# Optimization experiments

Measured on AMD Instinct MI355X. Metric: run time of the kernel, lower is better.

Reference implementation:

```python
import jax, jax.numpy as jnp
import numpy as np

N_NODES = 20000
N_EDGES = 640000
IN_FEAT = 128
OUT_FEAT = 128
NUM_RELS = 16


def setup_inputs() -> dict:
    key = jax.random.key(0)
    k_h, k_w, k_n, k_s, k_d, k_r = jax.random.split(key, 6)
    h = jax.random.normal(k_h, (N_NODES, IN_FEAT), dtype=jnp.float32)
    weight = jax.random.normal(k_w, (NUM_RELS, IN_FEAT, OUT_FEAT), dtype=jnp.float32)
    norm = jax.random.uniform(k_n, (N_EDGES, 1), dtype=jnp.float32)
    src = jax.random.randint(k_s, (N_EDGES,), 0, N_NODES, dtype=jnp.int32)
    dst = jax.random.randint(k_d, (N_EDGES,), 0, N_NODES, dtype=jnp.int32)
    rel_type = jax.random.randint(k_r, (N_EDGES,), 0, NUM_RELS, dtype=jnp.int32)
    return {"h": h, "weight": weight, "norm": norm,
            "src": src, "dst": dst, "rel_type": rel_type}


def reference(h, weight, norm, src, dst, rel_type):
    # Math of the non-input-layer path:
    #   msg_e = (h[src_e] @ weight[rel_e]) * norm_e ; h'_v = relu(sum_{e: dst_e=v} msg_e)
    # Efficient form: project node features through every relation once
    # (R*N*d*d flops, avoids materializing [E, d, d] gathered weights),
    # then gather the (rel, src) projection per edge.
    proj = jnp.einsum('nd,rde->rne', h, weight)      # [R, N, out]
    msg = proj[rel_type, src] * norm                 # [E, out]
    agg = jax.ops.segment_sum(msg, dst, num_segments=h.shape[0])  # [N, out]
    return jax.nn.relu(agg)
```

## Files before the change

### kernel.cpp

```cpp
#include <hip/hip_runtime.h>
#include <hip/hip_bf16.h>

#define FEAT 128
#define NRELS 16
#define BKT_SZ 32
#define PCHUNK 2048
#define CAP 2048

using short8 = __attribute__((ext_vector_type(8))) short;
using f32x4  = __attribute__((ext_vector_type(4))) float;

__device__ inline ushort f2bf(float x) {
    union { float f; unsigned int u; } v; v.f = x;
    unsigned int u = v.u;
    unsigned int r = (u + 0x7fffu + ((u >> 16) & 1u)) >> 16;
    return (ushort)r;
}
__device__ inline float bf2f(ushort b) {
    union { unsigned int u; float f; } v; v.u = ((unsigned int)b) << 16;
    return v.f;
}

__global__ __launch_bounds__(256) void prep_kernel(
    const float* __restrict__ h, const float* __restrict__ W,
    ushort* __restrict__ hpack, ushort* __restrict__ wpack,
    int* __restrict__ gcur,
    int n_nodes, int nmblk, int nbkt)
{
    const int bid = blockIdx.x;
    if (bid < nmblk) {
        int t = bid * 256 + threadIdx.x;
        int lane = t & 63;
        int mblk = t >> 8;
        int ks   = (t >> 6) & 3;
        int row  = mblk * 16 + (lane & 15);
        int k0   = ks * 32 + (lane >> 4) * 8;

        ushort u[8] = {0, 0, 0, 0, 0, 0, 0, 0};
        if (row < n_nodes) {
            const float* p = h + (size_t)row * FEAT + k0;
            float4 a = *reinterpret_cast<const float4*>(p);
            float4 b = *reinterpret_cast<const float4*>(p + 4);
            u[0] = f2bf(a.x); u[1] = f2bf(a.y); u[2] = f2bf(a.z); u[3] = f2bf(a.w);
            u[4] = f2bf(b.x); u[5] = f2bf(b.y); u[6] = f2bf(b.z); u[7] = f2bf(b.w);
        }
        *reinterpret_cast<short8*>(hpack + (size_t)t * 8) = *reinterpret_cast<short8*>(u);
    } else if (bid < nmblk + 128) {
        int t = (bid - nmblk) * 256 + threadIdx.x;
        int lane = t & 63;
        int ks   = (t >> 6) & 3;
        int fb   = (t >> 8) & 7;
        int r    = t >> 11;
        int k0   = ks * 32 + (lane >> 4) * 8;
        int f    = fb * 16 + (lane & 15);

        ushort u[8];
        #pragma unroll
        for (int j = 0; j < 8; ++j)
            u[j] = f2bf(W[((size_t)r * FEAT + (k0 + j)) * FEAT + f]);
        *reinterpret_cast<short8*>(wpack + (size_t)t * 8) = *reinterpret_cast<short8*>(u);
    } else {
        for (int i = threadIdx.x; i < nbkt + 1; i += 256) gcur[i] = 0;
    }
}

__global__ __launch_bounds__(256) void fused2_kernel(
    const ushort* __restrict__ hpack, const ushort* __restrict__ wpack,
    ushort* __restrict__ proj,
    const int* __restrict__ src, const int* __restrict__ dst,
    const int* __restrict__ rel, const float* __restrict__ norm,
    int* __restrict__ gcur, uint2* __restrict__ rtmp, int* __restrict__ ovf,
    int n_nodes, int nmblk, int n_edges, int nbkt, int nchunks)
{
    __shared__ __align__(16) char smem[32768];

    if ((int)blockIdx.x < nchunks) {
        int*    cnt   = (int*)smem;
        int*    base  = cnt + 1024;
        int*    cur   = base + 1024;
        uint2*  stage = (uint2*)(cur + 1024);
        ushort* sbkt  = (ushort*)(stage + PCHUNK);

        const int tid = threadIdx.x;
        const int c0 = blockIdx.x * PCHUNK;
        int* ovf_cnt = gcur + nbkt;

        for (int i = tid; i < nbkt; i += 256) { cnt[i] = 0; cur[i] = 0; }
        __syncthreads();

        #pragma unroll
        for (int j = 0; j < PCHUNK / 256; ++j) {
            int slot = j * 256 + tid;
            int e = c0 + slot;
            if (e < n_edges) {
                int d = dst[e];
                int b = d >> 5;
                uint2 r;
                r.x = (unsigned)src[e] | ((unsigned)rel[e] << 15) | ((unsigned)(d & 31) << 19);
                r.y = __float_as_uint(norm[e]);
                stage[slot] = r;
                sbkt[slot] = (ushort)b;
                atomicAdd(&cnt[b], 1);
            } else {
                sbkt[slot] = 0xffffu;
            }
        }
        __syncthreads();

        for (int i = tid; i < nbkt; i += 256)
            if (cnt[i] > 0) base[i] = atomicAdd(&gcur[i], cnt[i]);
        __syncthreads();

        #pragma unroll
        for (int j = 0; j < PCHUNK / 256; ++j) {
            int slot = j * 256 + tid;
            ushort b = sbkt[slot];
            if (b != 0xffffu) {
                int rank = atomicAdd(&cur[b], 1);
                int pos = base[b] + rank;
                if (pos < CAP)
                    rtmp[(size_t)b * CAP + pos] = stage[slot];
                else
                    ovf[atomicAdd(ovf_cnt, 1)] = c0 + slot;
            }
        }
    } else {
        const int bid2 = (int)blockIdx.x - nchunks;
        const int rr   = bid2 >> 7;
        const int bx   = bid2 & 127;

        const int lane = threadIdx.x & 63;
        const int wv   = threadIdx.x >> 6;
        ushort (*S)[136] = reinterpret_cast<ushort(*)[136]>(smem + wv * (16 * 136 * 2));

        const short8* wp = reinterpret_cast<const short8*>(wpack);
        const short8* hp = reinterpret_cast<const short8*>(hpack);

        short8 X[8][4];
        #pragma unroll
        for (int fb = 0; fb < 8; ++fb)
            #pragma unroll
            for (int ks = 0; ks < 4; ++ks)
                X[fb][ks] = wp[(((rr * 8 + fb) * 4 + ks) << 6) + lane];

        const int niter = (nmblk + 3) / 4;

        for (int it = bx; it < niter; it += 128) {
            const int mb = it * 4 + wv;
            const bool active = (mb < nmblk);

            f32x4 acc[8];
            #pragma unroll
            for (int fb = 0; fb < 8; ++fb) acc[fb] = f32x4{0.f, 0.f, 0.f, 0.f};

            if (active) {
                short8 Y[4];
                #pragma unroll
                for (int ks = 0; ks < 4; ++ks)
                    Y[ks] = hp[((mb * 4 + ks) << 6) + lane];

                #pragma unroll
                for (int ks = 0; ks < 4; ++ks)
                    #pragma unroll
                    for (int fb = 0; fb < 8; ++fb)
                        acc[fb] = __builtin_amdgcn_mfma_f32_16x16x32_bf16(X[fb][ks], Y[ks], acc[fb], 0, 0, 0);
            }

            __syncthreads();

            if (active) {
                #pragma unroll
                for (int fb = 0; fb < 8; ++fb) {
                    uint2 d;
                    d.x = (unsigned)f2bf(acc[fb][0]) | ((unsigned)f2bf(acc[fb][1]) << 16);
                    d.y = (unsigned)f2bf(acc[fb][2]) | ((unsigned)f2bf(acc[fb][3]) << 16);
                    *reinterpret_cast<uint2*>(&S[lane & 15][fb * 16 + (lane >> 4) * 4]) = d;
                }
            }

            __syncthreads();

            if (active) {
                #pragma unroll
                for (int i = 0; i < 4; ++i) {
                    const int row  = i * 4 + (lane >> 4);
                    const int node = mb * 16 + row;
                    if (node < n_nodes) {
                        uint4 v = *reinterpret_cast<const uint4*>(&S[row][(lane & 15) * 8]);
                        *reinterpret_cast<uint4*>(
                            proj + ((size_t)rr * n_nodes + node) * FEAT + (lane & 15) * 8) = v;
                    }
                }
            }
        }
    }
}

__global__ __launch_bounds__(512) void bgather_kernel(
    const ushort* __restrict__ proj, const uint2* __restrict__ rtmp,
    const int* __restrict__ gcur, const int* __restrict__ ovf,
    const int* __restrict__ src, const int* __restrict__ dst,
    const int* __restrict__ rel, const float* __restrict__ norm,
    float* __restrict__ out, int n_nodes, int nbkt)
{
    __shared__ uint2 stage[CAP];
    __shared__ uint2 sorted[CAP];
    __shared__ int cnt[BKT_SZ], cur[BKT_SZ], nbeg[BKT_SZ];

    const int b   = blockIdx.x;
    const int tid = threadIdx.x;
    const uint2* slab = rtmp + (size_t)b * CAP;

    const int total = gcur[b];
    const int n = (total < CAP) ? total : CAP;

    if (tid < BKT_SZ) cnt[tid] = 0;
    __syncthreads();
    for (int i = tid; i < n; i += 512) {
        uint2 r = slab[i];
        stage[i] = r;
        atomicAdd(&cnt[(r.x >> 19) & 31u], 1);
    }
    __syncthreads();
    if (tid == 0) {
        int run = 0;
        for (int k = 0; k < BKT_SZ; ++k) { nbeg[k] = run; cur[k] = run; run += cnt[k]; }
    }
    __syncthreads();
    for (int i = tid; i < n; i += 512) {
        uint2 r = stage[i];
        int p = atomicAdd(&cur[(r.x >> 19) & 31u], 1);
        sorted[p] = r;
    }
    __syncthreads();

    const int lane = tid & 63;
    const int wv   = tid >> 6;
    const int grp  = lane >> 4;
    const int sl   = lane & 15;
    const int k    = wv * 4 + grp;
    const int node = b * BKT_SZ + k;
    if (node >= n_nodes) return;

    float a0 = 0.f, a1 = 0.f, a2 = 0.f, a3 = 0.f;
    float a4 = 0.f, a5 = 0.f, a6 = 0.f, a7 = 0.f;

    const int s0 = nbeg[k];
    const int s1 = s0 + cnt[k];

    uint4 va, vb, vc;
    unsigned nm0 = 0, nm1 = 0, nm2 = 0;
    va = vb = vc = make_uint4(0u, 0u, 0u, 0u);
    if (s0 < s1) {
        uint2 r = sorted[s0]; nm0 = r.y;
        va = *reinterpret_cast<const uint4*>(proj +
            ((size_t)((r.x >> 15) & 0xfu) * n_nodes + (r.x & 0x7fffu)) * FEAT + sl * 8);
    }
    if (s0 + 1 < s1) {
        uint2 r = sorted[s0 + 1]; nm1 = r.y;
        vb = *reinterpret_cast<const uint4*>(proj +
            ((size_t)((r.x >> 15) & 0xfu) * n_nodes + (r.x & 0x7fffu)) * FEAT + sl * 8);
    }
    if (s0 + 2 < s1) {
        uint2 r = sorted[s0 + 2]; nm2 = r.y;
        vc = *reinterpret_cast<const uint4*>(proj +
            ((size_t)((r.x >> 15) & 0xfu) * n_nodes + (r.x & 0x7fffu)) * FEAT + sl * 8);
    }

    for (int s = s0; s < s1; ++s) {
        uint4 vcur = va; unsigned nmu = nm0;
        va = vb; nm0 = nm1;
        vb = vc; nm1 = nm2;
        if (s + 3 < s1) {
            uint2 r = sorted[s + 3]; nm2 = r.y;
            vc = *reinterpret_cast<const uint4*>(proj +
                ((size_t)((r.x >> 15) & 0xfu) * n_nodes + (r.x & 0x7fffu)) * FEAT + sl * 8);
        }
        float nmc = __uint_as_float(nmu);
        a0 += bf2f((ushort)(vcur.x & 0xffffu)) * nmc;
        a1 += bf2f((ushort)(vcur.x >> 16)) * nmc;
        a2 += bf2f((ushort)(vcur.y & 0xffffu)) * nmc;
        a3 += bf2f((ushort)(vcur.y >> 16)) * nmc;
        a4 += bf2f((ushort)(vcur.z & 0xffffu)) * nmc;
        a5 += bf2f((ushort)(vcur.z >> 16)) * nmc;
        a6 += bf2f((ushort)(vcur.w & 0xffffu)) * nmc;
        a7 += bf2f((ushort)(vcur.w >> 16)) * nmc;
    }

    const int novf = gcur[nbkt];
    for (int i = 0; i < novf; ++i) {
        int e = ovf[i];
        if (dst[e] == node) {
            float nmc = norm[e];
            const ushort* prow = proj +
                ((size_t)rel[e] * n_nodes + src[e]) * FEAT + sl * 8;
            uint4 v = *reinterpret_cast<const uint4*>(prow);
            a0 += bf2f((ushort)(v.x & 0xffffu)) * nmc;
            a1 += bf2f((ushort)(v.x >> 16)) * nmc;
            a2 += bf2f((ushort)(v.y & 0xffffu)) * nmc;
            a3 += bf2f((ushort)(v.y >> 16)) * nmc;
            a4 += bf2f((ushort)(v.z & 0xffffu)) * nmc;
            a5 += bf2f((ushort)(v.z >> 16)) * nmc;
            a6 += bf2f((ushort)(v.w & 0xffffu)) * nmc;
            a7 += bf2f((ushort)(v.w >> 16)) * nmc;
        }
    }

    float* o = out + (size_t)node * FEAT + sl * 8;
    float4 o0, o1;
    o0.x = fmaxf(a0, 0.f); o0.y = fmaxf(a1, 0.f);
    o0.z = fmaxf(a2, 0.f); o0.w = fmaxf(a3, 0.f);
    o1.x = fmaxf(a4, 0.f); o1.y = fmaxf(a5, 0.f);
    o1.z = fmaxf(a6, 0.f); o1.w = fmaxf(a7, 0.f);
    *reinterpret_cast<float4*>(o)     = o0;
    *reinterpret_cast<float4*>(o + 4) = o1;
}

constexpr int BM = 64;

__global__ __launch_bounds__(256) void proj_kernel(
    const float* __restrict__ h, const float* __restrict__ W,
    ushort* __restrict__ proj, int n_nodes, int r0)
{
    __shared__ ushort Wt[128][136];
    __shared__ ushort hs[BM][136];

    const int tid  = threadIdx.x;
    const int rel  = r0 + blockIdx.y;
    const float* Wg = W + (size_t)rel * FEAT * FEAT;

    #pragma unroll
    for (int it = 0; it < 16; ++it) {
        int f = (it * 256 + tid) * 4;
        int k = f >> 7, n = f & 127;
        float4 w4 = *reinterpret_cast<const float4*>(Wg + f);
        Wt[n + 0][k] = f2bf(w4.x);
        Wt[n + 1][k] = f2bf(w4.y);
        Wt[n + 2][k] = f2bf(w4.z);
        Wt[n + 3][k] = f2bf(w4.w);
    }

    const int lane = tid & 63;
    const int wave = tid >> 6;
    const int r    = lane & 15;
    const int kgrp = lane >> 4;

    ushort* projr = proj + (size_t)blockIdx.y * n_nodes * FEAT;
    const int nchunks = (n_nodes + BM - 1) / BM;

    for (int c = blockIdx.x; c < nchunks; c += gridDim.x) {
        const int m0 = c * BM;
        __syncthreads();
        #pragma unroll
        for (int it = 0; it < 8; ++it) {
            int f = (it * 256 + tid) * 4;
            int m = f >> 7, k = f & 127;
            int row = m0 + m;
            float4 v = make_float4(0.f, 0.f, 0.f, 0.f);
            if (row < n_nodes)
                v = *reinterpret_cast<const float4*>(h + (size_t)row * FEAT + k);
            ushort4 u;
            u.x = f2bf(v.x); u.y = f2bf(v.y); u.z = f2bf(v.z); u.w = f2bf(v.w);
            *reinterpret_cast<ushort4*>(&hs[m][k]) = u;
        }
        __syncthreads();

        f32x4 acc[8];
        #pragma unroll
        for (int i = 0; i < 8; ++i) acc[i] = f32x4{0.f, 0.f, 0.f, 0.f};

        #pragma unroll
        for (int kk = 0; kk < 4; ++kk) {
            const int kbase = kk * 32 + kgrp * 8;
            short8 a = *reinterpret_cast<const short8*>(&hs[wave * 16 + r][kbase]);
            #pragma unroll
            for (int ct = 0; ct < 8; ++ct) {
                short8 b = *reinterpret_cast<const short8*>(&Wt[ct * 16 + r][kbase]);
                acc[ct] = __builtin_amdgcn_mfma_f32_16x16x32_bf16(a, b, acc[ct], 0, 0, 0);
            }
        }

        #pragma unroll
        for (int ct = 0; ct < 8; ++ct) {
            #pragma unroll
            for (int i = 0; i < 4; ++i) {
                int row = m0 + wave * 16 + kgrp * 4 + i;
                if (row < n_nodes)
                    projr[(size_t)row * FEAT + ct * 16 + r] = f2bf(acc[ct][i]);
            }
        }
    }
}

__global__ __launch_bounds__(256) void edge_kernel(
    const ushort* __restrict__ proj, const float* __restrict__ norm,
    const int* __restrict__ src, const int* __restrict__ dst,
    const int* __restrict__ rel, float* __restrict__ out,
    int n_edges, int n_nodes, int r0, int r1)
{
    const int lane = threadIdx.x & 63;
    int gw = (int)((blockIdx.x * blockDim.x + threadIdx.x) >> 6);
    const int nw = (int)((gridDim.x * blockDim.x) >> 6);

    for (int e = gw; e < n_edges; e += nw) {
        int rr = rel[e];
        if (rr < r0 || rr >= r1) continue;
        int s = src[e];
        int d = dst[e];
        float nm = norm[e];
        const ushort* prow = proj + ((size_t)(rr - r0) * n_nodes + s) * FEAT;
        unsigned int v = *reinterpret_cast<const unsigned int*>(prow + lane * 2);
        float x0 = bf2f((ushort)(v & 0xffffu)) * nm;
        float x1 = bf2f((ushort)(v >> 16)) * nm;
        float* o = out + (size_t)d * FEAT + lane * 2;
        atomicAdd(o + 0, x0);
        atomicAdd(o + 1, x1);
    }
}

__global__ __launch_bounds__(256) void relu_kernel(float4* out, int n4)
{
    int i = blockIdx.x * blockDim.x + threadIdx.x;
    int stride = gridDim.x * blockDim.x;
    for (; i < n4; i += stride) {
        float4 v = out[i];
        v.x = fmaxf(v.x, 0.f);
        v.y = fmaxf(v.y, 0.f);
        v.z = fmaxf(v.z, 0.f);
        v.w = fmaxf(v.w, 0.f);
        out[i] = v;
    }
}

extern "C" void kernel_launch(void* const* d_in, const int* in_sizes, int n_in,
                              void* d_out, int out_size, void* d_ws, size_t ws_size,
                              hipStream_t stream)
{
    const float* h    = (const float*)d_in[0];
    const float* W    = (const float*)d_in[1];
    const float* norm = (const float*)d_in[2];
    const int*   src  = (const int*)d_in[3];
    const int*   dst  = (const int*)d_in[4];
    const int*   rel  = (const int*)d_in[5];
    float* out = (float*)d_out;

    const int n_nodes = in_sizes[0] / FEAT;
    const int n_edges = in_sizes[3];
    const int nmblk   = (n_nodes + 15) / 16;
    const int nbkt    = (n_nodes + BKT_SZ - 1) / BKT_SZ;
    const int nchunks = (n_edges + PCHUNK - 1) / PCHUNK;

    const size_t projB    = (size_t)NRELS * n_nodes * FEAT * sizeof(ushort);
    const size_t rtmpOff  = (projB + 255) & ~(size_t)255;
    const size_t rtmpB    = (size_t)nbkt * CAP * sizeof(uint2);
    const size_t ovfOff   = (rtmpOff + rtmpB + 255) & ~(size_t)255;
    const size_t ovfB     = (size_t)n_edges * sizeof(int);
    const size_t gcurOff  = (ovfOff + ovfB + 255) & ~(size_t)255;
    const size_t gcurB    = ((size_t)(nbkt + 1) * 4 + 255) & ~(size_t)255;
    const size_t hpackOff = gcurOff + gcurB;
    const size_t hpackB   = ((size_t)nmblk * 256 * 8 * sizeof(ushort) + 255) & ~(size_t)255;
    const size_t wpackOff = hpackOff + hpackB;
    const size_t wpackB   = (size_t)NRELS * 8 * 4 * 64 * 8 * sizeof(ushort);
    const size_t need     = wpackOff + wpackB;

    if (ws_size >= need && n_nodes < 32768 && nbkt <= 1024) {
        ushort* proj   = (ushort*)d_ws;
        uint2*  rtmp   = (uint2*)((char*)d_ws + rtmpOff);
        int*    ovf    = (int*)((char*)d_ws + ovfOff);
        int*    gcur   = (int*)((char*)d_ws + gcurOff);
        ushort* hpack  = (ushort*)((char*)d_ws + hpackOff);
        ushort* wpack  = (ushort*)((char*)d_ws + wpackOff);

        prep_kernel<<<nmblk + 128 + 1, 256, 0, stream>>>(
            h, W, hpack, wpack, gcur, n_nodes, nmblk, nbkt);

        fused2_kernel<<<nchunks + NRELS * 128, 256, 0, stream>>>(
            hpack, wpack, proj, src, dst, rel, norm, gcur, rtmp, ovf,
            n_nodes, nmblk, n_edges, nbkt, nchunks);

        bgather_kernel<<<nbkt, 512, 0, stream>>>(
            proj, rtmp, gcur, ovf, src, dst, rel, norm, out, n_nodes, nbkt);
    } else {
        ushort* proj = (ushort*)d_ws;
        hipMemsetAsync(out, 0, (size_t)out_size * sizeof(float), stream);
        const size_t perRel = (size_t)n_nodes * FEAT * sizeof(ushort);
        int rc = (int)(ws_size / perRel);
        if (rc < 1) rc = 1;
        if (rc > NRELS) rc = NRELS;
        for (int r0 = 0; r0 < NRELS; r0 += rc) {
            const int rcc = (rc < NRELS - r0) ? rc : (NRELS - r0);
            dim3 g1(32, rcc);
            proj_kernel<<<g1, 256, 0, stream>>>(h, W, proj, n_nodes, r0);
            edge_kernel<<<1024, 256, 0, stream>>>(proj, norm, src, dst, rel, out,
                                                  n_edges, n_nodes, r0, r0 + rcc);
        }
        relu_kernel<<<2048, 256, 0, stream>>>((float4*)out, out_size / 4);
    }
}
```

Before: 78.67 us.

## Split projection across waves by feature block and drop smem edge staging

The projection part now has all four waves of a block share one 16-node block, each computing two of the eight feature blocks. This cuts per-wave weight registers from 32 to 8 short8 vectors and shrinks shared memory to 12KB, which should allow more blocks per CU. The edge-partition part no longer stages edges in shared memory. It counts buckets in one pass and re-reads the edges from global memory in a second pass to scatter them, with a chunk of 8192 edges per block instead of 2048. The trade-off is a second global read of dst, and more loop iterations with two barriers each in the projection.

```diff
diff --git a/kernel.cpp b/kernel.cpp
--- a/kernel.cpp
+++ b/kernel.cpp
@@ -4,8 +4,9 @@
 #define FEAT 128
 #define NRELS 16
 #define BKT_SZ 32
-#define PCHUNK 2048
+#define PCHUNK 8192
 #define CAP 2048
+#define NB 128
 
 using short8 = __attribute__((ext_vector_type(8))) short;
 using f32x4  = __attribute__((ext_vector_type(4))) float;
@@ -72,14 +73,12 @@
     int* __restrict__ gcur, uint2* __restrict__ rtmp, int* __restrict__ ovf,
     int n_nodes, int nmblk, int n_edges, int nbkt, int nchunks)
 {
-    __shared__ __align__(16) char smem[32768];
+    __shared__ __align__(16) char smem[12288];
 
     if ((int)blockIdx.x < nchunks) {
-        int*    cnt   = (int*)smem;
-        int*    base  = cnt + 1024;
-        int*    cur   = base + 1024;
-        uint2*  stage = (uint2*)(cur + 1024);
-        ushort* sbkt  = (ushort*)(stage + PCHUNK);
+        int* cnt  = (int*)smem;
+        int* base = cnt + 1024;
+        int* cur  = base + 1024;
 
         const int tid = threadIdx.x;
         const int c0 = blockIdx.x * PCHUNK;
@@ -88,109 +87,90 @@
         for (int i = tid; i < nbkt; i += 256) { cnt[i] = 0; cur[i] = 0; }
         __syncthreads();
 
-        #pragma unroll
+        #pragma unroll 4
         for (int j = 0; j < PCHUNK / 256; ++j) {
-            int slot = j * 256 + tid;
-            int e = c0 + slot;
+            int e = c0 + j * 256 + tid;
+            if (e < n_edges) atomicAdd(&cnt[dst[e] >> 5], 1);
+        }
+        __syncthreads();
+
+        for (int i = tid; i < nbkt; i += 256)
+            if (cnt[i] > 0) base[i] = atomicAdd(&gcur[i], cnt[i]);
+        __syncthreads();
+
+        #pragma unroll 4
+        for (int j = 0; j < PCHUNK / 256; ++j) {
+            int e = c0 + j * 256 + tid;
             if (e < n_edges) {
                 int d = dst[e];
                 int b = d >> 5;
                 uint2 r;
                 r.x = (unsigned)src[e] | ((unsigned)rel[e] << 15) | ((unsigned)(d & 31) << 19);
                 r.y = __float_as_uint(norm[e]);
-                stage[slot] = r;
-                sbkt[slot] = (ushort)b;
-                atomicAdd(&cnt[b], 1);
-            } else {
-                sbkt[slot] = 0xffffu;
-            }
-        }
-        __syncthreads();
-
-        for (int i = tid; i < nbkt; i += 256)
-            if (cnt[i] > 0) base[i] = atomicAdd(&gcur[i], cnt[i]);
-        __syncthreads();
-
-        #pragma unroll
-        for (int j = 0; j < PCHUNK / 256; ++j) {
-            int slot = j * 256 + tid;
-            ushort b = sbkt[slot];
-            if (b != 0xffffu) {
                 int rank = atomicAdd(&cur[b], 1);
                 int pos = base[b] + rank;
                 if (pos < CAP)
-                    rtmp[(size_t)b * CAP + pos] = stage[slot];
+                    rtmp[(size_t)b * CAP + pos] = r;
                 else
-                    ovf[atomicAdd(ovf_cnt, 1)] = c0 + slot;
+                    ovf[atomicAdd(ovf_cnt, 1)] = e;
             }
         }
     } else {
         const int bid2 = (int)blockIdx.x - nchunks;
         const int rr   = bid2 >> 7;
-        const int bx   = bid2 & 127;
+        const int bx   = bid2 & (NB - 1);
 
         const int lane = threadIdx.x & 63;
         const int wv   = threadIdx.x >> 6;
-        ushort (*S)[136] = reinterpret_cast<ushort(*)[136]>(smem + wv * (16 * 136 * 2));
+        ushort (*S)[136] = reinterpret_cast<ushort(*)[136]>(smem);
 
         const short8* wp = reinterpret_cast<const short8*>(wpack);
         const short8* hp = reinterpret_cast<const short8*>(hpack);
 
-        short8 X[8][4];
-        #pragma unroll
-        for (int fb = 0; fb < 8; ++fb)
+        short8 X[2][4];
+        #pragma unroll
+        for (int fbl = 0; fbl < 2; ++fbl)
             #pragma unroll
             for (int ks = 0; ks < 4; ++ks)
-                X[fb][ks] = wp[(((rr * 8 + fb) * 4 + ks) << 6) + lane];
-
-        const int niter = (nmblk + 3) / 4;
-
-        for (int it = bx; it < niter; it += 128) {
-            const int mb = it * 4 + wv;
-            const bool active = (mb < nmblk);
-
-            f32x4 acc[8];
-            #pragma unroll
-            for (int fb = 0; fb < 8; ++fb) acc[fb] = f32x4{0.f, 0.f, 0.f, 0.f};
-
-            if (active) {
-                short8 Y[4];
-                #pragma unroll
-                for (int ks = 0; ks < 4; ++ks)
-                    Y[ks] = hp[((mb * 4 + ks) << 6) + lane];
-
-                #pragma unroll
-                for (int ks = 0; ks < 4; ++ks)
-                    #pragma unroll
-                    for (int fb = 0; fb < 8; ++fb)
-                        acc[fb] = __builtin_amdgcn_mfma_f32_16x16x32_bf16(X[fb][ks], Y[ks], acc[fb], 0, 0, 0);
+                X[fbl][ks] = wp[(((rr * 8 + wv * 2 + fbl) * 4 + ks) << 6) + lane];
+
+        const int srow = threadIdx.x >> 4;
+        const int sc16 = threadIdx.x & 15;
+
+        for (int mb = bx; mb < nmblk; mb += NB) {
+            short8 Y[4];
+            #pragma unroll
+            for (int ks = 0; ks < 4; ++ks)
+                Y[ks] = hp[((mb * 4 + ks) << 6) + lane];
+
+            f32x4 acc[2];
+            acc[0] = f32x4{0.f, 0.f, 0.f, 0.f};
+            acc[1] = f32x4{0.f, 0.f, 0.f, 0.f};
+
+            #pragma unroll
+            for (int ks = 0; ks < 4; ++ks) {
+                acc[0] = __builtin_amdgcn_mfma_f32_16x16x32_bf16(X[0][ks], Y[ks], acc[0], 0, 0, 0);
+                acc[1] = __builtin_amdgcn_mfma_f32_16x16x32_bf16(X[1][ks], Y[ks], acc[1], 0, 0, 0);
             }
 
             __syncthreads();
 
-            if (active) {
-                #pragma unroll
-                for (int fb = 0; fb < 8; ++fb) {
-                    uint2 d;
-                    d.x = (unsigned)f2bf(acc[fb][0]) | ((unsigned)f2bf(acc[fb][1]) << 16);
-                    d.y = (unsigned)f2bf(acc[fb][2]) | ((unsigned)f2bf(acc[fb][3]) << 16);
-                    *reinterpret_cast<uint2*>(&S[lane & 15][fb * 16 + (lane >> 4) * 4]) = d;
-                }
+            #pragma unroll
+            for (int fbl = 0; fbl < 2; ++fbl) {
+                const int fb = wv * 2 + fbl;
+                uint2 d;
+                d.x = (unsigned)f2bf(acc[fbl][0]) | ((unsigned)f2bf(acc[fbl][1]) << 16);
+                d.y = (unsigned)f2bf(acc[fbl][2]) | ((unsigned)f2bf(acc[fbl][3]) << 16);
+                *reinterpret_cast<uint2*>(&S[lane & 15][fb * 16 + (lane >> 4) * 4]) = d;
             }
 
             __syncthreads();
 
-            if (active) {
-                #pragma unroll
-                for (int i = 0; i < 4; ++i) {
-                    const int row  = i * 4 + (lane >> 4);
-                    const int node = mb * 16 + row;
-                    if (node < n_nodes) {
-                        uint4 v = *reinterpret_cast<const uint4*>(&S[row][(lane & 15) * 8]);
-                        *reinterpret_cast<uint4*>(
-                            proj + ((size_t)rr * n_nodes + node) * FEAT + (lane & 15) * 8) = v;
-                    }
-                }
+            const int node = mb * 16 + srow;
+            if (node < n_nodes) {
+                uint4 v = *reinterpret_cast<const uint4*>(&S[srow][sc16 * 8]);
+                *reinterpret_cast<uint4*>(
+                    proj + ((size_t)rr * n_nodes + node) * FEAT + sc16 * 8) = v;
             }
         }
     }
@@ -474,7 +454,7 @@
         prep_kernel<<<nmblk + 128 + 1, 256, 0, stream>>>(
             h, W, hpack, wpack, gcur, n_nodes, nmblk, nbkt);
 
-        fused2_kernel<<<nchunks + NRELS * 128, 256, 0, stream>>>(
+        fused2_kernel<<<nchunks + NRELS * NB, 256, 0, stream>>>(
             hpack, wpack, proj, src, dst, rel, norm, gcur, rtmp, ovf,
             n_nodes, nmblk, n_edges, nbkt, nchunks);
 
```

Result: slower. 82.14 us (+4.4%).
